# Performance work log

Measured on AMD Instinct MI355X. Metric: run time of the kernel, lower is better.

The kernel has to match this reference:

```python
import jax, jax.numpy as jnp
import numpy as np

B, C_IN, L = 4, 512, 16384
C_RED = C_IN // 2  # q/k/v reduced channels = 256
BL = 64            # sliding-window block size
NEG = -jnp.inf


def setup_inputs() -> dict:
    key = jax.random.key(0)
    ks = jax.random.split(key, 8)
    x1 = jax.random.normal(ks[0], (B, C_IN, L), dtype=jnp.float32)
    x2 = jax.random.normal(ks[1], (B, C_IN, L), dtype=jnp.float32)
    mask = jnp.ones((B, 1, L), dtype=jnp.float32)
    s = 0.02
    Wq = jax.random.normal(ks[2], (C_RED, C_IN), dtype=jnp.float32) * s
    Wk = jax.random.normal(ks[3], (C_RED, C_IN), dtype=jnp.float32) * s
    Wv = jax.random.normal(ks[4], (C_RED, C_IN), dtype=jnp.float32) * s
    Wo = jax.random.normal(ks[5], (C_IN, C_RED), dtype=jnp.float32) * s
    bq = jnp.zeros((C_RED,), jnp.float32)
    bk = jnp.zeros((C_RED,), jnp.float32)
    bv = jnp.zeros((C_RED,), jnp.float32)
    bo = jnp.zeros((C_IN,), jnp.float32)
    return {"x1": x1, "x2": x2, "mask": mask, "Wq": Wq, "bq": bq,
            "Wk": Wk, "bk": bk, "Wv": Wv, "bv": bv, "Wo": Wo, "bo": bo}


def _conv1x1(W, b, x):
    # x: (B, Cin, L) -> (B, Cout, L)
    return jnp.einsum('oc,bcl->bol', W, x) + b[None, :, None]


def reference(x1, x2, mask, Wq, bq, Wk, bk, Wv, bv, Wo, bo):
    # encoder stage: value comes from x1 (x2 unused)
    q = _conv1x1(Wq, bq, x1)  # (B, C, L)
    k = _conv1x1(Wk, bk, x1)
    v = _conv1x1(Wv, bv, x1)

    Bq, C, Lq = q.shape
    bl = BL
    nb = (Lq + bl - 1) // bl
    pad = nb * bl - Lq
    if pad > 0:
        q = jnp.pad(q, ((0, 0), (0, 0), (0, pad)))
        k = jnp.pad(k, ((0, 0), (0, 0), (0, pad)))
        v = jnp.pad(v, ((0, 0), (0, 0), (0, pad)))
        mask = jnp.pad(mask, ((0, 0), (0, 0), (0, pad)))

    # non-overlapping windows: (B, C, nb, bl)
    qb = q.reshape(Bq, C, nb, bl)
    kb = k.reshape(Bq, C, nb, bl)
    vb = v.reshape(Bq, C, nb, bl)
    mb = mask.reshape(Bq, 1, nb, bl)  # (B,1,nb,bl)

    scale = 1.0 / jnp.sqrt(jnp.float32(C))
    # per-block attention scores: (B, nb, bl_i, bl_j)
    scores = jnp.einsum('bcni,bcnj->bnij', qb, kb) * scale
    key_mask = mb[:, 0, :, None, :]  # (B, nb, 1, bl_j)
    scores = jnp.where(key_mask == 0, NEG, scores)
    probs = jax.nn.softmax(scores, axis=-1)
    attn = jnp.einsum('bnij,bcnj->bcni', probs, vb)  # (B, C, nb, bl)

    h = jax.nn.relu(attn)
    out = jnp.einsum('oc,bcni->boni', Wo, h) + bo[None, :, None, None]
    out = out.reshape(Bq, Wo.shape[0], nb * bl)
    if pad > 0:
        out = out[:, :, :Lq]
    return out
```

## Files before the change

kernel.cpp:

```cpp
#include <hip/hip_runtime.h>
#include <hip/hip_fp16.h>
#include <stdint.h>

#define BB    4
#define CIN   512
#define CRED  256
#define LL    16384
#define NBLK  256
#define WELEM 131072

typedef _Float16 half8 __attribute__((ext_vector_type(8)));
typedef float    f32x4 __attribute__((ext_vector_type(4)));

#define SWZ(r) (((r)&7)<<4)

#define QB      524288
#define KB      (QB + 16777216)
#define VB      (KB + 16777216)
#define WS_NEED ((size_t)(VB + 16777216) * 2)

__global__ void convert_weights_fm(const float* __restrict__ Wq,
                                   const float* __restrict__ Wk,
                                   const float* __restrict__ Wv,
                                   const float* __restrict__ Wo,
                                   _Float16* __restrict__ dst) {
    int i = blockIdx.x * blockDim.x + threadIdx.x;
    int p = i >> 17;
    int e17 = i & (WELEM - 1);
    const float* src = (p == 0) ? Wq : (p == 1) ? Wk : (p == 2) ? Wv : Wo;
    const int Kd = (p < 3) ? 512 : 256;
    const int sh = (p < 3) ? 13 : 12;
    const int m16 = e17 >> sh;
    const int rem = e17 & ((1 << sh) - 1);
    const int ks  = rem >> 9;
    const int l4  = (rem >> 7) & 3;
    const int l15 = (rem >> 3) & 15;
    const int ee  = rem & 7;
    const int r = m16 * 16 + l15;
    const int k = ks * 32 + l4 * 8 + ee;
    dst[(size_t)p * WELEM + e17] = (_Float16)src[(size_t)r * Kd + k];
}

__global__ void convert_weights_rm(const float* __restrict__ Wq,
                                   const float* __restrict__ Wk,
                                   const float* __restrict__ Wv,
                                   const float* __restrict__ Wo,
                                   _Float16* __restrict__ dst) {
    int i = blockIdx.x * blockDim.x + threadIdx.x;
    int m = i >> 17;
    int e = i & (WELEM - 1);
    const float* src = (m == 0) ? Wq : (m == 1) ? Wk : (m == 2) ? Wv : Wo;
    dst[(size_t)m * WELEM + e] = (_Float16)src[e];
}

__global__ __launch_bounds__(256, 3)
void qkv_v4(const float* __restrict__ x1, const _Float16* __restrict__ W,
            const float* __restrict__ bq, const float* __restrict__ bk,
            const float* __restrict__ bv, _Float16* __restrict__ ws) {
    __shared__ _Float16 bt[2][4096];
    const int tid = threadIdx.x;
    const int wid = tid >> 6;
    const int l15 = tid & 15;
    const int l4  = (tid & 63) >> 4;
    const int p   = blockIdx.x >> 10;
    const int t   = blockIdx.x & 1023;
    const int b   = t >> 8, n = t & 255;

    const int c4 = tid & 15;
    const int pq = tid >> 4;
    const float* xb = x1 + ((size_t)b * CIN + 4 * c4) * LL + n * 64 + 4 * pq;
    const int sH  = c4 >> 3;
    const int l4b = (c4 >> 1) & 3;
    const int e0  = (c4 & 1) * 4;

    f32x4 st[4];
    #define X_ISSUE(KT) do {                                                  \
        _Pragma("unroll")                                                     \
        for (int i_ = 0; i_ < 4; ++i_)                                        \
            st[i_] = *(const f32x4*)(xb + (size_t)((KT) * 64 + i_) * LL);     \
    } while (0)
    #define X_COMMIT(BUF) do {                                                \
        _Pragma("unroll")                                                     \
        for (int u_ = 0; u_ < 4; ++u_) {                                      \
            union { _Float16 h[4]; uint64_t q; } pk_;                         \
            _Pragma("unroll")                                                 \
            for (int i_ = 0; i_ < 4; ++i_) pk_.h[i_] = (_Float16)st[i_][u_];  \
            *(uint64_t*)(&bt[BUF][sH * 2048 + l4b * 512 + (4 * pq + u_) * 8 + e0]) = pk_.q; \
        }                                                                     \
    } while (0)

    X_ISSUE(0);
    X_COMMIT(0);
    __syncthreads();

    f32x4 acc[4][4];
    #pragma unroll
    for (int mt = 0; mt < 4; ++mt)
        #pragma unroll
        for (int q = 0; q < 4; ++q) acc[mt][q] = (f32x4){0.f, 0.f, 0.f, 0.f};

    const _Float16* wf0 = W + (size_t)p * WELEM + (size_t)(wid * 4) * 8192
                        + l4 * 128 + l15 * 8;

    #pragma unroll
    for (int kt = 0; kt < 8; ++kt) {
        const int cur = kt & 1;
        if (kt < 7) X_ISSUE(kt + 1);
        #pragma unroll
        for (int s = 0; s < 2; ++s) {
            const int ks = kt * 2 + s;
            half8 xf[4], wf[4];
            #pragma unroll
            for (int nt = 0; nt < 4; ++nt)
                xf[nt] = *(const half8*)(&bt[cur][s * 2048 + l4 * 512 + (nt * 16 + l15) * 8]);
            #pragma unroll
            for (int mt = 0; mt < 4; ++mt)
                wf[mt] = *(const half8*)(wf0 + mt * 8192 + ks * 512);
            #pragma unroll
            for (int mt = 0; mt < 4; ++mt)
                #pragma unroll
                for (int nt = 0; nt < 4; ++nt)
                    acc[mt][nt] = __builtin_amdgcn_mfma_f32_16x16x32_f16(
                        wf[mt], xf[nt], acc[mt][nt], 0, 0, 0);
        }
        if (kt < 7) X_COMMIT(cur ^ 1);
        __syncthreads();
    }
    #undef X_ISSUE
    #undef X_COMMIT

    const float* bias = (p == 0) ? bq : (p == 1) ? bk : bv;
    if (p < 2) {
        _Float16* dst = ws + (p ? KB : QB) + ((size_t)b * LL + n * 64) * CRED;
        #pragma unroll
        for (int mt = 0; mt < 4; ++mt) {
            const int c0 = wid * 64 + mt * 16 + l4 * 4;
            f32x4 b4 = *(const f32x4*)(bias + c0);
            #pragma unroll
            for (int nt = 0; nt < 4; ++nt) {
                const int pos = nt * 16 + l15;
                union { _Float16 h[4]; uint64_t q; } pk;
                #pragma unroll
                for (int ri = 0; ri < 4; ++ri)
                    pk.h[ri] = (_Float16)(acc[mt][nt][ri] + b4[ri]);
                *(uint64_t*)(dst + (size_t)pos * CRED + c0) = pk.q;
            }
        }
    } else {
        _Float16* vd = ws + VB + (size_t)b * CRED * LL + n * 64;
        #pragma unroll
        for (int mt = 0; mt < 4; ++mt) {
            const int c0 = wid * 64 + mt * 16 + l4 * 4;
            f32x4 b4 = *(const f32x4*)(bias + c0);
            #pragma unroll
            for (int nt = 0; nt < 4; ++nt) {
                const int pos = nt * 16 + l15;
                #pragma unroll
                for (int ri = 0; ri < 4; ++ri)
                    vd[(size_t)(c0 + ri) * LL + pos] =
                        (_Float16)(acc[mt][nt][ri] + b4[ri]);
            }
        }
    }
}

#define BH_OFF 0
#define BP_OFF 32768
#define LDS_B  40960

__global__ __launch_bounds__(256, 3)
void attn_out(const float* __restrict__ mask, const _Float16* __restrict__ ws,
              const float* __restrict__ bo, float* __restrict__ out) {
    extern __shared__ char lds[];
    const int tid = threadIdx.x;
    const int wid = tid >> 6;
    const int l15 = tid & 15;
    const int l4  = (tid & 63) >> 4;
    const int b   = blockIdx.x >> 8;
    const int n   = blockIdx.x & 255;

    const _Float16* qt = ws + QB + ((size_t)b * LL + n * 64) * CRED;
    const _Float16* kt = ws + KB + ((size_t)b * LL + n * 64) * CRED;
    const _Float16* vt = ws + VB + (size_t)b * CRED * LL + n * 64;
    const _Float16* WoF = ws + 3 * (size_t)WELEM;

    {
        const int i0 = wid * 16;
        f32x4 sa[4];
        #pragma unroll
        for (int jt = 0; jt < 4; ++jt) sa[jt] = (f32x4){0.f, 0.f, 0.f, 0.f};
        #pragma unroll
        for (int ks = 0; ks < 8; ++ks) {
            half8 qa = *(const half8*)(qt + (size_t)(i0 + l15) * CRED + ks * 32 + l4 * 8);
            #pragma unroll
            for (int jt = 0; jt < 4; ++jt) {
                half8 kf = *(const half8*)(kt + (size_t)(jt * 16 + l15) * CRED + ks * 32 + l4 * 8);
                sa[jt] = __builtin_amdgcn_mfma_f32_16x16x32_f16(qa, kf, sa[jt], 0, 0, 0);
            }
        }
        float msk[4];
        #pragma unroll
        for (int jt = 0; jt < 4; ++jt)
            msk[jt] = mask[(size_t)b * LL + n * 64 + jt * 16 + l15];
        #pragma unroll
        for (int ri = 0; ri < 4; ++ri) {
            float v[4];
            #pragma unroll
            for (int jt = 0; jt < 4; ++jt)
                v[jt] = (msk[jt] == 0.f) ? -1e30f : sa[jt][ri] * 0.0625f;
            float mx = fmaxf(fmaxf(v[0], v[1]), fmaxf(v[2], v[3]));
            mx = fmaxf(mx, __shfl_xor(mx, 1));
            mx = fmaxf(mx, __shfl_xor(mx, 2));
            mx = fmaxf(mx, __shfl_xor(mx, 4));
            mx = fmaxf(mx, __shfl_xor(mx, 8));
            float e[4], sum = 0.f;
            #pragma unroll
            for (int jt = 0; jt < 4; ++jt) { e[jt] = __expf(v[jt] - mx); sum += e[jt]; }
            sum += __shfl_xor(sum, 1);
            sum += __shfl_xor(sum, 2);
            sum += __shfl_xor(sum, 4);
            sum += __shfl_xor(sum, 8);
            const float inv = 1.f / sum;
            const int i = i0 + l4 * 4 + ri;
            #pragma unroll
            for (int jt = 0; jt < 4; ++jt) {
                const int j = jt * 16 + l15;
                *(_Float16*)(lds + BP_OFF + i * 128 + ((2 * j) ^ SWZ(i))) =
                    (_Float16)(e[jt] * inv);
            }
        }
    }
    __syncthreads();

    {
        const int cb = wid * 64;
        f32x4 pv[4][4];
        #pragma unroll
        for (int m = 0; m < 4; ++m)
            #pragma unroll
            for (int q = 0; q < 4; ++q) pv[m][q] = (f32x4){0.f, 0.f, 0.f, 0.f};
        #pragma unroll
        for (int ks = 0; ks < 2; ++ks) {
            const int kb = ks * 64 + l4 * 16;
            half8 pb[4];
            #pragma unroll
            for (int nt = 0; nt < 4; ++nt) {
                const int i = nt * 16 + l15;
                pb[nt] = *(const half8*)(lds + BP_OFF + i * 128 + (kb ^ SWZ(i)));
            }
            #pragma unroll
            for (int mt = 0; mt < 4; ++mt) {
                half8 va = *(const half8*)(vt + (size_t)(cb + mt * 16 + l15) * LL + ks * 32 + l4 * 8);
                #pragma unroll
                for (int nt = 0; nt < 4; ++nt)
                    pv[mt][nt] = __builtin_amdgcn_mfma_f32_16x16x32_f16(va, pb[nt], pv[mt][nt], 0, 0, 0);
            }
        }
        #pragma unroll
        for (int mt = 0; mt < 4; ++mt) {
            const int c0 = cb + mt * 16 + l4 * 4;
            #pragma unroll
            for (int nt = 0; nt < 4; ++nt) {
                const int j = nt * 16 + l15;
                union { _Float16 h[4]; uint64_t q; } hp;
                #pragma unroll
                for (int ri = 0; ri < 4; ++ri)
                    hp.h[ri] = (_Float16)fmaxf(pv[mt][nt][ri], 0.f);
                *(uint64_t*)(lds + BH_OFF + j * 512 + ((2 * c0) ^ SWZ(j))) = hp.q;
            }
        }
    }
    __syncthreads();

    #pragma unroll
    for (int op = 0; op < 2; ++op) {
        const int mbo = wid * 128 + op * 64;
        f32x4 oa[4][4];
        #pragma unroll
        for (int m = 0; m < 4; ++m)
            #pragma unroll
            for (int q = 0; q < 4; ++q) oa[m][q] = (f32x4){0.f, 0.f, 0.f, 0.f};
        const _Float16* wof = WoF + (size_t)(wid * 8 + op * 4) * 4096 + l4 * 128 + l15 * 8;
        #pragma unroll 4
        for (int ks = 0; ks < 8; ++ks) {
            const int kb = ks * 64 + l4 * 16;
            half8 hb[4];
            #pragma unroll
            for (int nt = 0; nt < 4; ++nt) {
                const int i = nt * 16 + l15;
                hb[nt] = *(const half8*)(lds + BH_OFF + i * 512 + (kb ^ SWZ(i)));
            }
            #pragma unroll
            for (int mt = 0; mt < 4; ++mt) {
                half8 wa = *(const half8*)(wof + mt * 4096 + ks * 512);
                #pragma unroll
                for (int nt = 0; nt < 4; ++nt)
                    oa[mt][nt] = __builtin_amdgcn_mfma_f32_16x16x32_f16(wa, hb[nt], oa[mt][nt], 0, 0, 0);
            }
        }
        #pragma unroll
        for (int mt = 0; mt < 4; ++mt) {
            const int o0 = mbo + mt * 16 + l4 * 4;
            f32x4 bov = *(const f32x4*)(bo + o0);
            #pragma unroll
            for (int ri = 0; ri < 4; ++ri) {
                float* orow = out + ((size_t)b * CIN + (o0 + ri)) * LL + n * 64;
                #pragma unroll
                for (int nt = 0; nt < 4; ++nt)
                    orow[nt * 16 + l15] = oa[mt][nt][ri] + bov[ri];
            }
        }
    }
}

#define XT_OFF 0
#define Q_OFF  0
#define K_OFF  32768
#define V_OFF  32768
#define H_OFF  0
#define P_OFF  65536
#define MSK_OFF 73728
#define LDS_BYTES 73984

__global__ __launch_bounds__(256, 2)
void att_fused(const float* __restrict__ x1, const float* __restrict__ mask,
               const _Float16* __restrict__ W,
               const float* __restrict__ bq, const float* __restrict__ bk,
               const float* __restrict__ bv, const float* __restrict__ bo,
               float* __restrict__ out) {
    extern __shared__ char lds[];
    const int tid  = threadIdx.x;
    const int wid  = tid >> 6;
    const int lane = tid & 63;
    const int l15  = lane & 15;
    const int l4   = lane >> 4;
    const int blk  = blockIdx.x;
    const int b    = blk >> 8;
    const int n    = blk & 255;

    const _Float16* Wq = W;
    const _Float16* Wk = W + WELEM;
    const _Float16* Wv = W + 2 * WELEM;
    const _Float16* Wo = W + 3 * WELEM;

    {
        const int jx = tid & 15;
        const int rb = tid >> 4;
        const float* xbase = x1 + ((size_t)b * CIN + 2 * rb) * LL + n * 64 + 4 * jx;
        #pragma unroll
        for (int i = 0; i < 16; ++i) {
            f32x4 a = *(const f32x4*)(xbase + (size_t)(32 * i) * LL);
            f32x4 c = *(const f32x4*)(xbase + (size_t)(32 * i + 1) * LL);
            const int col = 4 * rb + 64 * i;
            #pragma unroll
            for (int u = 0; u < 4; ++u) {
                union { _Float16 h[2]; uint32_t w; } p;
                p.h[0] = (_Float16)a[u];
                p.h[1] = (_Float16)c[u];
                const int j = 4 * jx + u;
                *(uint32_t*)(lds + XT_OFF + j * 1024 + (col ^ SWZ(j))) = p.w;
            }
        }
        if (tid < 64)
            *(float*)(lds + MSK_OFF + tid * 4) = mask[(size_t)b * LL + n * 64 + tid];
    }
    __syncthreads();

    uint64_t qh[4][4], kh[4][4], vh[4][4];
    #pragma unroll
    for (int pass = 0; pass < 4; ++pass) {
        f32x4 aQ[4], aK[4], aV[4];
        #pragma unroll
        for (int q = 0; q < 4; ++q) {
            aQ[q] = (f32x4){0.f, 0.f, 0.f, 0.f};
            aK[q] = (f32x4){0.f, 0.f, 0.f, 0.f};
            aV[q] = (f32x4){0.f, 0.f, 0.f, 0.f};
        }
        const int mrow = wid * 64 + pass * 16 + l15;
        const _Float16* wqp = Wq + (size_t)mrow * CIN + l4 * 8;
        const _Float16* wkp = Wk + (size_t)mrow * CIN + l4 * 8;
        const _Float16* wvp = Wv + (size_t)mrow * CIN + l4 * 8;
        #pragma unroll 4
        for (int ks = 0; ks < 16; ++ks) {
            const int kb = ks * 64 + l4 * 16;
            half8 xb[4];
            #pragma unroll
            for (int nt = 0; nt < 4; ++nt) {
                const int j = nt * 16 + l15;
                xb[nt] = *(const half8*)(lds + XT_OFF + j * 1024 + (kb ^ SWZ(j)));
            }
            half8 aq = *(const half8*)(wqp + ks * 32);
            half8 ak = *(const half8*)(wkp + ks * 32);
            half8 av = *(const half8*)(wvp + ks * 32);
            #pragma unroll
            for (int nt = 0; nt < 4; ++nt) {
                aQ[nt] = __builtin_amdgcn_mfma_f32_16x16x32_f16(aq, xb[nt], aQ[nt], 0, 0, 0);
                aK[nt] = __builtin_amdgcn_mfma_f32_16x16x32_f16(ak, xb[nt], aK[nt], 0, 0, 0);
                aV[nt] = __builtin_amdgcn_mfma_f32_16x16x32_f16(av, xb[nt], aV[nt], 0, 0, 0);
            }
        }
        const int c0 = wid * 64 + pass * 16 + l4 * 4;
        f32x4 bqv = *(const f32x4*)(bq + c0);
        f32x4 bkv = *(const f32x4*)(bk + c0);
        f32x4 bvv = *(const f32x4*)(bv + c0);
        #pragma unroll
        for (int nt = 0; nt < 4; ++nt) {
            union { _Float16 h[4]; uint64_t q; } qp, kp, vp;
            #pragma unroll
            for (int ri = 0; ri < 4; ++ri) {
                qp.h[ri] = (_Float16)(aQ[nt][ri] + bqv[ri]);
                kp.h[ri] = (_Float16)(aK[nt][ri] + bkv[ri]);
                vp.h[ri] = (_Float16)(aV[nt][ri] + bvv[ri]);
            }
            qh[pass][nt] = qp.q;
            kh[pass][nt] = kp.q;
            vh[pass][nt] = vp.q;
        }
    }
    __syncthreads();

    #pragma unroll
    for (int pass = 0; pass < 4; ++pass) {
        const int c0 = wid * 64 + pass * 16 + l4 * 4;
        #pragma unroll
        for (int nt = 0; nt < 4; ++nt) {
            const int j = nt * 16 + l15;
            *(uint64_t*)(lds + Q_OFF + j * 512 + ((2 * c0) ^ SWZ(j))) = qh[pass][nt];
            *(uint64_t*)(lds + K_OFF + j * 512 + ((2 * c0) ^ SWZ(j))) = kh[pass][nt];
        }
    }
    __syncthreads();

    {
        const int i0 = wid * 16;
        f32x4 sa[4];
        #pragma unroll
        for (int jt = 0; jt < 4; ++jt) sa[jt] = (f32x4){0.f, 0.f, 0.f, 0.f};
        #pragma unroll
        for (int ks = 0; ks < 8; ++ks) {
            const int kb = ks * 64 + l4 * 16;
            const int iq = i0 + l15;
            half8 qa = *(const half8*)(lds + Q_OFF + iq * 512 + (kb ^ SWZ(iq)));
            #pragma unroll
            for (int jt = 0; jt < 4; ++jt) {
                const int jr = jt * 16 + l15;
                half8 kf = *(const half8*)(lds + K_OFF + jr * 512 + (kb ^ SWZ(jr)));
                sa[jt] = __builtin_amdgcn_mfma_f32_16x16x32_f16(qa, kf, sa[jt], 0, 0, 0);
            }
        }
        float msk[4];
        #pragma unroll
        for (int jt = 0; jt < 4; ++jt)
            msk[jt] = *(const float*)(lds + MSK_OFF + (jt * 16 + l15) * 4);
        #pragma unroll
        for (int ri = 0; ri < 4; ++ri) {
            float v[4];
            #pragma unroll
            for (int jt = 0; jt < 4; ++jt)
                v[jt] = (msk[jt] == 0.f) ? -1e30f : sa[jt][ri] * 0.0625f;
            float mx = fmaxf(fmaxf(v[0], v[1]), fmaxf(v[2], v[3]));
            mx = fmaxf(mx, __shfl_xor(mx, 1));
            mx = fmaxf(mx, __shfl_xor(mx, 2));
            mx = fmaxf(mx, __shfl_xor(mx, 4));
            mx = fmaxf(mx, __shfl_xor(mx, 8));
            float e[4], sum = 0.f;
            #pragma unroll
            for (int jt = 0; jt < 4; ++jt) { e[jt] = __expf(v[jt] - mx); sum += e[jt]; }
            sum += __shfl_xor(sum, 1);
            sum += __shfl_xor(sum, 2);
            sum += __shfl_xor(sum, 4);
            sum += __shfl_xor(sum, 8);
            const float inv = 1.f / sum;
            const int i = i0 + l4 * 4 + ri;
            #pragma unroll
            for (int jt = 0; jt < 4; ++jt) {
                const int j = jt * 16 + l15;
                *(_Float16*)(lds + P_OFF + i * 128 + ((2 * j) ^ SWZ(i))) =
                    (_Float16)(e[jt] * inv);
            }
        }
    }
    __syncthreads();

    #pragma unroll
    for (int pass = 0; pass < 4; ++pass) {
        const int c0 = wid * 64 + pass * 16 + l4 * 4;
        #pragma unroll
        for (int nt = 0; nt < 4; ++nt) {
            const int j = nt * 16 + l15;
            const uint64_t v64 = vh[pass][nt];
            #pragma unroll
            for (int ri = 0; ri < 4; ++ri) {
                const int c = c0 + ri;
                *(uint16_t*)(lds + V_OFF + c * 128 + ((2 * j) ^ SWZ(c))) =
                    (uint16_t)(v64 >> (16 * ri));
            }
        }
    }
    __syncthreads();

    {
        const int cb = wid * 64;
        f32x4 pv[4][4];
        #pragma unroll
        for (int m = 0; m < 4; ++m)
            #pragma unroll
            for (int q = 0; q < 4; ++q) pv[m][q] = (f32x4){0.f, 0.f, 0.f, 0.f};
        #pragma unroll
        for (int ks = 0; ks < 2; ++ks) {
            const int kb = ks * 64 + l4 * 16;
            half8 pb[4];
            #pragma unroll
            for (int nt = 0; nt < 4; ++nt) {
                const int i = nt * 16 + l15;
                pb[nt] = *(const half8*)(lds + P_OFF + i * 128 + (kb ^ SWZ(i)));
            }
            #pragma unroll
            for (int mt = 0; mt < 4; ++mt) {
                const int c = cb + mt * 16 + l15;
                half8 va = *(const half8*)(lds + V_OFF + c * 128 + (kb ^ SWZ(c)));
                #pragma unroll
                for (int nt = 0; nt < 4; ++nt)
                    pv[mt][nt] = __builtin_amdgcn_mfma_f32_16x16x32_f16(va, pb[nt], pv[mt][nt], 0, 0, 0);
            }
        }
        #pragma unroll
        for (int mt = 0; mt < 4; ++mt) {
            const int c0 = cb + mt * 16 + l4 * 4;
            #pragma unroll
            for (int nt = 0; nt < 4; ++nt) {
                const int j = nt * 16 + l15;
                union { _Float16 h[4]; uint64_t q; } hp;
                #pragma unroll
                for (int ri = 0; ri < 4; ++ri)
                    hp.h[ri] = (_Float16)fmaxf(pv[mt][nt][ri], 0.f);
                *(uint64_t*)(lds + H_OFF + j * 512 + ((2 * c0) ^ SWZ(j))) = hp.q;
            }
        }
    }
    __syncthreads();

    #pragma unroll
    for (int op = 0; op < 2; ++op) {
        const int mbo = wid * 128 + op * 64;
        const _Float16* wob = Wo + (size_t)(mbo + l15) * CRED + l4 * 8;
        f32x4 oa[4][4];
        #pragma unroll
        for (int m = 0; m < 4; ++m)
            #pragma unroll
            for (int q = 0; q < 4; ++q) oa[m][q] = (f32x4){0.f, 0.f, 0.f, 0.f};
        #pragma unroll 4
        for (int ks = 0; ks < 8; ++ks) {
            const int kb = ks * 64 + l4 * 16;
            half8 hb[4];
            #pragma unroll
            for (int nt = 0; nt < 4; ++nt) {
                const int i = nt * 16 + l15;
                hb[nt] = *(const half8*)(lds + H_OFF + i * 512 + (kb ^ SWZ(i)));
            }
            #pragma unroll
            for (int mt = 0; mt < 4; ++mt) {
                half8 wa = *(const half8*)(wob + mt * 16 * CRED + ks * 32);
                #pragma unroll
                for (int nt = 0; nt < 4; ++nt)
                    oa[mt][nt] = __builtin_amdgcn_mfma_f32_16x16x32_f16(wa, hb[nt], oa[mt][nt], 0, 0, 0);
            }
        }
        #pragma unroll
        for (int mt = 0; mt < 4; ++mt) {
            const int o0 = mbo + mt * 16 + l4 * 4;
            f32x4 bov = *(const f32x4*)(bo + o0);
            #pragma unroll
            for (int ri = 0; ri < 4; ++ri) {
                float* orow = out + ((size_t)b * CIN + (o0 + ri)) * LL + n * 64;
                #pragma unroll
                for (int nt = 0; nt < 4; ++nt)
                    orow[nt * 16 + l15] = oa[mt][nt][ri] + bov[ri];
            }
        }
    }
}

extern "C" void kernel_launch(void* const* d_in, const int* in_sizes, int n_in,
                              void* d_out, int out_size, void* d_ws, size_t ws_size,
                              hipStream_t stream) {
    const float* x1   = (const float*)d_in[0];
    const float* mask = (const float*)d_in[2];
    const float* Wq   = (const float*)d_in[3];
    const float* bq   = (const float*)d_in[4];
    const float* Wk   = (const float*)d_in[5];
    const float* bk   = (const float*)d_in[6];
    const float* Wv   = (const float*)d_in[7];
    const float* bv   = (const float*)d_in[8];
    const float* Wo   = (const float*)d_in[9];
    const float* bo   = (const float*)d_in[10];
    float* out = (float*)d_out;
    _Float16* wbuf = (_Float16*)d_ws;

    if (ws_size >= WS_NEED) {
        convert_weights_fm<<<2048, 256, 0, stream>>>(Wq, Wk, Wv, Wo, wbuf);
        qkv_v4<<<3 * BB * NBLK, 256, 0, stream>>>(x1, wbuf, bq, bk, bv, wbuf);
        attn_out<<<BB * NBLK, 256, LDS_B, stream>>>(mask, wbuf, bo, out);
    } else {
        convert_weights_rm<<<2048, 256, 0, stream>>>(Wq, Wk, Wv, Wo, wbuf);
        (void)hipFuncSetAttribute((const void*)att_fused,
                                  hipFuncAttributeMaxDynamicSharedMemorySize, LDS_BYTES);
        att_fused<<<BB * NBLK, 256, LDS_BYTES, stream>>>(x1, mask, wbuf, bq, bk, bv, bo, out);
    }
}
```

Measured before the change: 173.2 us.

## Pre-transpose x1 to fp16 fragment layout and use blocked V layout

Adds an x_transpose kernel that converts x1 to fp16 in an MFMA-fragment-friendly tiled layout, so the QKV projection kernel reads X fragments straight from global memory instead of staging through LDS with double buffering. Previously each of the three projections converted x1 separately; now the conversion happens once, done in two batch halves so the fp16 buffer stays small and cache-friendly. V is also stored per 64-token tile (channel x 64) rather than strided by L, which makes the attention kernel's V reads contiguous. The cost is an extra kernel launch pair and an extra fp16 round trip of x through memory.

```diff
diff --git a/kernel.cpp b/kernel.cpp
--- a/kernel.cpp
+++ b/kernel.cpp
@@ -14,9 +14,10 @@
 
 #define SWZ(r) (((r)&7)<<4)
 
-#define QB      524288
-#define KB      (QB + 16777216)
-#define VB      (KB + 16777216)
+#define XFH     524288
+#define QB      (XFH + 16777216)
+#define KB      (QB  + 16777216)
+#define VB      (KB  + 16777216)
 #define WS_NEED ((size_t)(VB + 16777216) * 2)
 
 __global__ void convert_weights_fm(const float* __restrict__ Wq,
@@ -53,85 +54,84 @@
     dst[(size_t)m * WELEM + e] = (_Float16)src[e];
 }
 
+__global__ __launch_bounds__(256, 4)
+void x_transpose(const float* __restrict__ x1, _Float16* __restrict__ xfb,
+                 int b0) {
+    __shared__ char lds[16384];
+    const int tid = threadIdx.x;
+    const int blk = blockIdx.x;
+    const int tl  = blk >> 2;
+    const int cc  = blk & 3;
+    const int b   = b0 + (tl >> 8), n = tl & 255;
+    const int jx  = tid & 15;
+    const int rg  = tid >> 4;
+
+    const float* xp = x1 + ((size_t)b * CIN + cc * 128 + 8 * rg) * LL + n * 64 + 4 * jx;
+    f32x4 r[8];
+    #pragma unroll
+    for (int k = 0; k < 8; ++k)
+        r[k] = *(const f32x4*)(xp + (size_t)k * LL);
+    asm volatile("" ::: "memory");
+    #pragma unroll
+    for (int u = 0; u < 4; ++u) {
+        const int j = 4 * jx + u;
+        union { _Float16 h[8]; half8 v; } pk;
+        #pragma unroll
+        for (int k = 0; k < 8; ++k) pk.h[k] = (_Float16)r[k][u];
+        *(half8*)(lds + j * 256 + ((16 * rg) ^ SWZ(j))) = pk.v;
+    }
+    __syncthreads();
+    _Float16* dst = xfb + (size_t)tl * 32768 + cc * 8192;
+    const int l4d = tid >> 6, jd = tid & 63;
+    #pragma unroll
+    for (int rr = 0; rr < 4; ++rr) {
+        half8 v = *(const half8*)(lds + jd * 256 + ((rr * 64 + l4d * 16) ^ SWZ(jd)));
+        *(half8*)(dst + rr * 2048 + tid * 8) = v;
+    }
+}
+
 __global__ __launch_bounds__(256, 3)
-void qkv_v4(const float* __restrict__ x1, const _Float16* __restrict__ W,
+void qkv_v5(const _Float16* __restrict__ W, const _Float16* __restrict__ xfb,
             const float* __restrict__ bq, const float* __restrict__ bk,
-            const float* __restrict__ bv, _Float16* __restrict__ ws) {
-    __shared__ _Float16 bt[2][4096];
+            const float* __restrict__ bv, _Float16* __restrict__ ws, int b0) {
     const int tid = threadIdx.x;
     const int wid = tid >> 6;
     const int l15 = tid & 15;
     const int l4  = (tid & 63) >> 4;
-    const int p   = blockIdx.x >> 10;
-    const int t   = blockIdx.x & 1023;
-    const int b   = t >> 8, n = t & 255;
-
-    const int c4 = tid & 15;
-    const int pq = tid >> 4;
-    const float* xb = x1 + ((size_t)b * CIN + 4 * c4) * LL + n * 64 + 4 * pq;
-    const int sH  = c4 >> 3;
-    const int l4b = (c4 >> 1) & 3;
-    const int e0  = (c4 & 1) * 4;
-
-    f32x4 st[4];
-    #define X_ISSUE(KT) do {                                                  \
-        _Pragma("unroll")                                                     \
-        for (int i_ = 0; i_ < 4; ++i_)                                        \
-            st[i_] = *(const f32x4*)(xb + (size_t)((KT) * 64 + i_) * LL);     \
-    } while (0)
-    #define X_COMMIT(BUF) do {                                                \
-        _Pragma("unroll")                                                     \
-        for (int u_ = 0; u_ < 4; ++u_) {                                      \
-            union { _Float16 h[4]; uint64_t q; } pk_;                         \
-            _Pragma("unroll")                                                 \
-            for (int i_ = 0; i_ < 4; ++i_) pk_.h[i_] = (_Float16)st[i_][u_];  \
-            *(uint64_t*)(&bt[BUF][sH * 2048 + l4b * 512 + (4 * pq + u_) * 8 + e0]) = pk_.q; \
-        }                                                                     \
-    } while (0)
-
-    X_ISSUE(0);
-    X_COMMIT(0);
-    __syncthreads();
-
-    f32x4 acc[4][4];
-    #pragma unroll
-    for (int mt = 0; mt < 4; ++mt)
-        #pragma unroll
-        for (int q = 0; q < 4; ++q) acc[mt][q] = (f32x4){0.f, 0.f, 0.f, 0.f};
-
+    const int p   = blockIdx.x >> 9;
+    const int tl  = blockIdx.x & 511;
+    const size_t tg = (size_t)b0 * 256 + tl;
+
+    const _Float16* xf  = xfb + (size_t)tl * 32768;
     const _Float16* wf0 = W + (size_t)p * WELEM + (size_t)(wid * 4) * 8192
                         + l4 * 128 + l15 * 8;
 
-    #pragma unroll
-    for (int kt = 0; kt < 8; ++kt) {
-        const int cur = kt & 1;
-        if (kt < 7) X_ISSUE(kt + 1);
-        #pragma unroll
-        for (int s = 0; s < 2; ++s) {
-            const int ks = kt * 2 + s;
-            half8 xf[4], wf[4];
+    f32x4 acc[4][4];
+    #pragma unroll
+    for (int mt = 0; mt < 4; ++mt)
+        #pragma unroll
+        for (int q = 0; q < 4; ++q) acc[mt][q] = (f32x4){0.f, 0.f, 0.f, 0.f};
+
+    #pragma unroll
+    for (int ks = 0; ks < 16; ++ks) {
+        half8 xfr[4], wfr[4];
+        #pragma unroll
+        for (int nt = 0; nt < 4; ++nt)
+            xfr[nt] = *(const half8*)(xf + ks * 2048 + l4 * 512 + (nt * 16 + l15) * 8);
+        #pragma unroll
+        for (int mt = 0; mt < 4; ++mt)
+            wfr[mt] = *(const half8*)(wf0 + mt * 8192 + ks * 512);
+        #pragma unroll
+        for (int mt = 0; mt < 4; ++mt)
             #pragma unroll
             for (int nt = 0; nt < 4; ++nt)
-                xf[nt] = *(const half8*)(&bt[cur][s * 2048 + l4 * 512 + (nt * 16 + l15) * 8]);
-            #pragma unroll
-            for (int mt = 0; mt < 4; ++mt)
-                wf[mt] = *(const half8*)(wf0 + mt * 8192 + ks * 512);
-            #pragma unroll
-            for (int mt = 0; mt < 4; ++mt)
-                #pragma unroll
-                for (int nt = 0; nt < 4; ++nt)
-                    acc[mt][nt] = __builtin_amdgcn_mfma_f32_16x16x32_f16(
-                        wf[mt], xf[nt], acc[mt][nt], 0, 0, 0);
-        }
-        if (kt < 7) X_COMMIT(cur ^ 1);
-        __syncthreads();
-    }
-    #undef X_ISSUE
-    #undef X_COMMIT
+                acc[mt][nt] = __builtin_amdgcn_mfma_f32_16x16x32_f16(
+                    wfr[mt], xfr[nt], acc[mt][nt], 0, 0, 0);
+    }
 
     const float* bias = (p == 0) ? bq : (p == 1) ? bk : bv;
     if (p < 2) {
-        _Float16* dst = ws + (p ? KB : QB) + ((size_t)b * LL + n * 64) * CRED;
+        _Float16* dst = ws + (p ? KB : QB) + tg * 16384;
         #pragma unroll
         for (int mt = 0; mt < 4; ++mt) {
             const int c0 = wid * 64 + mt * 16 + l4 * 4;
@@ -147,7 +147,7 @@
             }
         }
     } else {
-        _Float16* vd = ws + VB + (size_t)b * CRED * LL + n * 64;
+        _Float16* vd = ws + VB + tg * 16384;
         #pragma unroll
         for (int mt = 0; mt < 4; ++mt) {
             const int c0 = wid * 64 + mt * 16 + l4 * 4;
@@ -157,7 +157,7 @@
                 const int pos = nt * 16 + l15;
                 #pragma unroll
                 for (int ri = 0; ri < 4; ++ri)
-                    vd[(size_t)(c0 + ri) * LL + pos] =
+                    vd[(size_t)(c0 + ri) * 64 + pos] =
                         (_Float16)(acc[mt][nt][ri] + b4[ri]);
             }
         }
@@ -176,12 +176,12 @@
     const int wid = tid >> 6;
     const int l15 = tid & 15;
     const int l4  = (tid & 63) >> 4;
-    const int b   = blockIdx.x >> 8;
-    const int n   = blockIdx.x & 255;
-
-    const _Float16* qt = ws + QB + ((size_t)b * LL + n * 64) * CRED;
-    const _Float16* kt = ws + KB + ((size_t)b * LL + n * 64) * CRED;
-    const _Float16* vt = ws + VB + (size_t)b * CRED * LL + n * 64;
+    const int t   = blockIdx.x;
+    const int b   = t >> 8, n = t & 255;
+
+    const _Float16* qt = ws + QB + (size_t)t * 16384;
+    const _Float16* kt = ws + KB + (size_t)t * 16384;
+    const _Float16* vt = ws + VB + (size_t)t * 16384;
     const _Float16* WoF = ws + 3 * (size_t)WELEM;
 
     {
@@ -250,7 +250,7 @@
             }
             #pragma unroll
             for (int mt = 0; mt < 4; ++mt) {
-                half8 va = *(const half8*)(vt + (size_t)(cb + mt * 16 + l15) * LL + ks * 32 + l4 * 8);
+                half8 va = *(const half8*)(vt + (size_t)(cb + mt * 16 + l15) * 64 + ks * 32 + l4 * 8);
                 #pragma unroll
                 for (int nt = 0; nt < 4; ++nt)
                     pv[mt][nt] = __builtin_amdgcn_mfma_f32_16x16x32_f16(va, pb[nt], pv[mt][nt], 0, 0, 0);
@@ -599,7 +599,11 @@
 
     if (ws_size >= WS_NEED) {
         convert_weights_fm<<<2048, 256, 0, stream>>>(Wq, Wk, Wv, Wo, wbuf);
-        qkv_v4<<<3 * BB * NBLK, 256, 0, stream>>>(x1, wbuf, bq, bk, bv, wbuf);
+        _Float16* xfb = wbuf + XFH;
+        for (int h = 0; h < 2; ++h) {
+            x_transpose<<<2048, 256, 0, stream>>>(x1, xfb, 2 * h);
+            qkv_v5<<<1536, 256, 0, stream>>>(wbuf, xfb, bq, bk, bv, wbuf, 2 * h);
+        }
         attn_out<<<BB * NBLK, 256, LDS_B, stream>>>(mask, wbuf, bo, out);
     } else {
         convert_weights_rm<<<2048, 256, 0, stream>>>(Wq, Wk, Wv, Wo, wbuf);
```

Result: slower. 211.7 us (+22.2%).
